# Kernel tuning notes

Measured on AMD Instinct MI355X. Metric: run time of the kernel, lower is better.

## Reference

```python
import jax, jax.numpy as jnp
import numpy as np

N, E, D, H, O = 100000, 1600000, 128, 128, 64
EPS = 1e-5


def setup_inputs() -> dict:
    key = jax.random.key(0)
    ks = jax.random.split(key, 12)
    s = 0.05
    return {
        "x": jax.random.normal(ks[0], (N, D), jnp.float32),
        "edge_index": jax.random.randint(ks[1], (2, E), 0, N),
        "W1": jax.random.normal(ks[2], (D, H), jnp.float32) * s,
        "b1": jnp.zeros((H,), jnp.float32),
        "W2": jax.random.normal(ks[3], (H, H), jnp.float32) * s,
        "b2": jnp.zeros((H,), jnp.float32),
        "W3": jax.random.normal(ks[4], (H, H), jnp.float32) * s,
        "b3": jnp.zeros((H,), jnp.float32),
        "g1": jnp.ones((H,), jnp.float32),
        "be1": jnp.zeros((H,), jnp.float32),
        "g2": jnp.ones((H,), jnp.float32),
        "be2": jnp.zeros((H,), jnp.float32),
        "Wp1": jax.random.normal(ks[5], (H, H), jnp.float32) * s,
        "bp1": jnp.zeros((H,), jnp.float32),
        "Wp2": jax.random.normal(ks[6], (H, O), jnp.float32) * s,
        "bp2": jnp.zeros((O,), jnp.float32),
    }


def _layer_norm(h, g, b):
    mu = jnp.mean(h, axis=-1, keepdims=True)
    var = jnp.mean(jnp.square(h - mu), axis=-1, keepdims=True)
    return g * (h - mu) * jax.lax.rsqrt(var + EPS) + b


def reference(x, edge_index, W1, b1, W2, b2, W3, b3, g1, be1, g2, be2, Wp1, bp1, Wp2, bp2):
    n = x.shape[0]
    loop = jnp.arange(n)
    # GCN: add self-loops, symmetric normalization D^-1/2 (A+I) D^-1/2
    src = jnp.concatenate([edge_index[0], loop])
    dst = jnp.concatenate([edge_index[1], loop])
    deg = jax.ops.segment_sum(jnp.ones_like(src, x.dtype), dst, num_segments=n)
    dinv = jax.lax.rsqrt(jnp.maximum(deg, 1e-12))
    norm = dinv[src] * dinv[dst]  # [E+N]

    def gcn_conv(h, W, b):
        hw = h @ W                              # transform first (PyG GCNConv)
        msg = hw[src] * norm[:, None]           # gather + edge scale
        return jax.ops.segment_sum(msg, dst, num_segments=n) + b  # scatter-add

    # dropout is a no-op in eval mode
    h = _layer_norm(jax.nn.relu(gcn_conv(x, W1, b1)), g1, be1)
    h = _layer_norm(jax.nn.relu(gcn_conv(h, W2, b2)), g2, be2)
    h = jax.nn.relu(gcn_conv(h, W3, b3))
    h = h @ Wp1 + bp1
    h = h @ Wp2 + bp2
    return jax.nn.sigmoid(h)
```

## Files before the change

kernel.cpp:

```cpp
#include <hip/hip_runtime.h>
#include <hip/hip_bf16.h>

typedef __attribute__((ext_vector_type(8))) short short8;
typedef __attribute__((ext_vector_type(4))) float floatx4;
typedef unsigned int u32;

__device__ __forceinline__ u32 f2bf(float f) {
    union { float f; u32 u; } c; c.f = f;
    return (c.u + 0x7FFFu + ((c.u >> 16) & 1u)) >> 16;
}

__device__ __forceinline__ void fp8x8_acc(uint2 v, float* a) {
    auto f0 = __builtin_amdgcn_cvt_pk_f32_fp8((int)v.x, false);
    auto f1 = __builtin_amdgcn_cvt_pk_f32_fp8((int)v.x, true);
    auto f2 = __builtin_amdgcn_cvt_pk_f32_fp8((int)v.y, false);
    auto f3 = __builtin_amdgcn_cvt_pk_f32_fp8((int)v.y, true);
    a[0] += ((const float*)&f0)[0]; a[1] += ((const float*)&f0)[1];
    a[2] += ((const float*)&f1)[0]; a[3] += ((const float*)&f1)[1];
    a[4] += ((const float*)&f2)[0]; a[5] += ((const float*)&f2)[1];
    a[6] += ((const float*)&f3)[0]; a[7] += ((const float*)&f3)[1];
}
__device__ __forceinline__ void fp8x8_dec(uint2 v, float* x) {
    auto f0 = __builtin_amdgcn_cvt_pk_f32_fp8((int)v.x, false);
    auto f1 = __builtin_amdgcn_cvt_pk_f32_fp8((int)v.x, true);
    auto f2 = __builtin_amdgcn_cvt_pk_f32_fp8((int)v.y, false);
    auto f3 = __builtin_amdgcn_cvt_pk_f32_fp8((int)v.y, true);
    x[0] = ((const float*)&f0)[0]; x[1] = ((const float*)&f0)[1];
    x[2] = ((const float*)&f1)[0]; x[3] = ((const float*)&f1)[1];
    x[4] = ((const float*)&f2)[0]; x[5] = ((const float*)&f2)[1];
    x[6] = ((const float*)&f3)[0]; x[7] = ((const float*)&f3)[1];
}
__device__ __forceinline__ u32 f32x4_to_fp8(float a, float b, float c, float d) {
    u32 w = (u32)__builtin_amdgcn_cvt_pk_fp8_f32(a, b, 0, false);
    w = (u32)__builtin_amdgcn_cvt_pk_fp8_f32(c, d, (int)w, true);
    return w;
}

#define CCAP 264
#define CAPB 8192

__device__ __forceinline__ void gatherq(const uint2* __restrict__ hw64,
                                        const int* __restrict__ col,
                                        int* __restrict__ ldsc,
                                        int begq, int endq, int beg, int stagelen,
                                        int lane, int s16, float* __restrict__ acc) {
    for (int i = lane; i < stagelen; i += 64) ldsc[i] = col[beg + i];
    __syncthreads();
    int dq = endq - begq;
    int offq = begq - beg;
    int send = min(endq, beg + stagelen);
    int sdq = max(0, send - begq);
    int mx = sdq;
    mx = max(mx, __shfl_xor(mx, 16));
    mx = max(mx, __shfl_xor(mx, 32));
    for (int jb = 0; jb < mx; jb += 8) {
        uint2 v[8];
#pragma unroll
        for (int j = 0; j < 8; ++j) {
            int jj = jb + j;
            int cj = ldsc[min(offq + jj, CCAP - 1)];
            bool act = jj < sdq;
            uint2 tv; tv.x = 0u; tv.y = 0u;
            if (act) tv = hw64[(size_t)cj * 16 + s16];
            v[j] = tv;
        }
#pragma unroll
        for (int j = 0; j < 8; ++j) fp8x8_acc(v[j], acc);
    }
    for (int j = sdq; j < dq; ++j) {
        int cj = col[begq + j];
        uint2 tv = hw64[(size_t)cj * 16 + s16];
        fp8x8_acc(tv, acc);
    }
}

__global__ __launch_bounds__(256) void bucket_trans_k(
        const int* __restrict__ src, const int* __restrict__ dst,
        int* __restrict__ gcnt, u32* __restrict__ pairs, int E, int nb, int bucketB,
        const float* __restrict__ W1, const float* __restrict__ W2,
        const float* __restrict__ W3, const float* __restrict__ Wp1,
        const float* __restrict__ Wp2,
        unsigned short* __restrict__ o1, unsigned short* __restrict__ o2,
        unsigned short* __restrict__ o3, unsigned short* __restrict__ o4,
        unsigned short* __restrict__ o5) {
    int t = threadIdx.x;
    if ((int)blockIdx.x >= bucketB) {
        int i = (blockIdx.x - bucketB) * 256 + t;
        const float* in; unsigned short* out; int cols, li;
        if (i < 16384)      { in = W1;  out = o1; cols = 128; li = i; }
        else if (i < 32768) { in = W2;  out = o2; cols = 128; li = i - 16384; }
        else if (i < 49152) { in = W3;  out = o3; cols = 128; li = i - 32768; }
        else if (i < 65536) { in = Wp1; out = o4; cols = 128; li = i - 49152; }
        else                { in = Wp2; out = o5; cols = 64;  li = i - 65536; }
        int r = li / cols, c = li - r * cols;
        out[(size_t)c * 128 + r] = (unsigned short)f2bf(in[li]);
        return;
    }
    __shared__ int cnt[512];
    __shared__ int gbase[512];
    __shared__ int cur[512];
    cnt[t] = 0; cnt[t + 256] = 0;
    __syncthreads();
    int e0 = blockIdx.x * 8192;
    int ne = min(8192, E - e0);
    for (int i = t; i < ne; i += 256) atomicAdd(&cnt[dst[e0 + i] >> 8], 1);
    __syncthreads();
    for (int b = t; b < nb; b += 256) {
        int c = cnt[b];
        gbase[b] = c ? (b * CAPB + atomicAdd(&gcnt[b], c)) : 0;
        cur[b] = 0;
    }
    __syncthreads();
    for (int i = t; i < ne; i += 256) {
        int d = dst[e0 + i];
        int s = src[e0 + i];
        int b = d >> 8;
        int p = atomicAdd(&cur[b], 1);
        pairs[gbase[b] + p] = (u32)s | ((u32)(d & 255) << 24);
    }
}

#define LCOL_CAP 12288
__global__ __launch_bounds__(256) void build_k(const u32* __restrict__ pairs,
                                               const int* __restrict__ gcnt,
                                               int* __restrict__ rowptr,
                                               float* __restrict__ dinv,
                                               int* __restrict__ col,
                                               int N, int E, int nb) {
    __shared__ int pre[512];
    __shared__ int cnt[256], incl[256], cur[256];
    __shared__ int lcol[LCOL_CAP];
    int b = blockIdx.x, t = threadIdx.x;
    pre[t] = (t < nb) ? gcnt[t] : 0;
    pre[t + 256] = (t + 256 < nb) ? gcnt[t + 256] : 0;
    __syncthreads();
    for (int off = 1; off < 512; off <<= 1) {
        int a0 = (t >= off) ? pre[t - off] : 0;
        int a1 = (t + 256 >= off) ? pre[t + 256 - off] : 0;
        __syncthreads();
        pre[t] += a0;
        pre[t + 256] += a1;
        __syncthreads();
    }
    int myg = gcnt[b];
    int base = pre[b] - myg;
    int sbase = b * CAPB;
    int ecnt = myg;
    cnt[t] = 0;
    __syncthreads();
    for (int j = t; j < ecnt; j += 256) atomicAdd(&cnt[pairs[sbase + j] >> 24], 1);
    __syncthreads();
    incl[t] = cnt[t];
    __syncthreads();
    for (int off = 1; off < 256; off <<= 1) {
        int a = (t >= off) ? incl[t - off] : 0;
        __syncthreads();
        incl[t] += a;
        __syncthreads();
    }
    int myc = cnt[t];
    int ex = incl[t] - myc;
    int node = b * 256 + t;
    if (node < N) {
        rowptr[node] = base + ex;
        dinv[node] = rsqrtf((float)myc + 1.0f);
    }
    cur[t] = ex;
    if (b == 0 && t == 0) rowptr[N] = E;
    __syncthreads();
    if (ecnt <= LCOL_CAP) {
        for (int j = t; j < ecnt; j += 256) {
            u32 v = pairs[sbase + j];
            int r = atomicAdd(&cur[v >> 24], 1);
            lcol[r] = (int)(v & 0xFFFFFF);
        }
        __syncthreads();
        for (int j = t; j < ecnt; j += 256) col[base + j] = lcol[j];
    } else {
        for (int j = t; j < ecnt; j += 256) {
            u32 v = pairs[sbase + j];
            int r = atomicAdd(&cur[v >> 24], 1);
            col[base + r] = (int)(v & 0xFFFFFF);
        }
    }
}

__global__ __launch_bounds__(256) void gemm1_k(const float* __restrict__ A,
                                               const short* __restrict__ Wt,
                                               const float* __restrict__ dinv,
                                               u32* __restrict__ out, int M) {
    __shared__ unsigned short xs[64][132];
    int t = threadIdx.x;
    int wave = t >> 6, lane = t & 63;
    int r0 = blockIdx.x * 64;
#pragma unroll
    for (int i = 0; i < 8; ++i) {
        int idx = i * 256 + t;
        int row = idx >> 5;
        int c4 = idx & 31;
        int grow = r0 + row;
        float4 f = {0.f, 0.f, 0.f, 0.f};
        if (grow < M) f = ((const float4*)A)[(size_t)grow * 32 + c4];
        uint2 bb;
        bb.x = f2bf(f.x) | (f2bf(f.y) << 16);
        bb.y = f2bf(f.z) | (f2bf(f.w) << 16);
        *(uint2*)&xs[row][c4 * 4] = bb;
    }
    __syncthreads();
    int m0 = r0 + wave * 16;
    if (m0 >= M) return;
    int quad = lane >> 4, lr = lane & 15;
    int lrow = wave * 16 + lr;
    int row = m0 + lr;
    bool wr = row < M;
    short8 b0 = *(const short8*)&xs[lrow][quad * 8];
    short8 b1 = *(const short8*)&xs[lrow][32 + quad * 8];
    short8 b2 = *(const short8*)&xs[lrow][64 + quad * 8];
    short8 b3 = *(const short8*)&xs[lrow][96 + quad * 8];
    float di = wr ? dinv[row] : 0.f;
#pragma unroll
    for (int nt = 0; nt < 8; ++nt) {
        int ncol = nt * 16 + lr;
        const short8* Wp = (const short8*)(Wt + (size_t)ncol * 128 + quad * 8);
        short8 a0 = Wp[0], a1 = Wp[4], a2 = Wp[8], a3 = Wp[12];
        floatx4 acc = {0.f, 0.f, 0.f, 0.f};
        acc = __builtin_amdgcn_mfma_f32_16x16x32_bf16(a0, b0, acc, 0, 0, 0);
        acc = __builtin_amdgcn_mfma_f32_16x16x32_bf16(a1, b1, acc, 0, 0, 0);
        acc = __builtin_amdgcn_mfma_f32_16x16x32_bf16(a2, b2, acc, 0, 0, 0);
        acc = __builtin_amdgcn_mfma_f32_16x16x32_bf16(a3, b3, acc, 0, 0, 0);
        if (wr) {
            out[(size_t)row * 32 + nt * 4 + quad] =
                f32x4_to_fp8(acc[0] * di, acc[1] * di, acc[2] * di, acc[3] * di);
        }
    }
}

__global__ __launch_bounds__(256) void fconv_k(const uint2* __restrict__ hw64,
                                               const int* __restrict__ rowptr,
                                               const int* __restrict__ col,
                                               const float* __restrict__ dinv,
                                               const float* __restrict__ bias,
                                               const float* __restrict__ gam,
                                               const float* __restrict__ bet,
                                               const short* __restrict__ Wt,
                                               u32* __restrict__ out, int N) {
    __shared__ unsigned short rows[16][136];
    __shared__ int ldsc[4][CCAP];
    int t = threadIdx.x, wave = t >> 6, lane = t & 63;
    int q = lane >> 4, s16 = lane & 15;
    int nb0 = blockIdx.x * 16;
    int node0 = nb0 + wave * 4;
    int node = node0 + q;
    bool ok = node < N;
    int beg = rowptr[min(node0, N)];
    int e4  = rowptr[min(node0 + 4, N)];
    int begq = rowptr[min(node, N)];
    int endq = ok ? rowptr[min(node + 1, N)] : begq;
    int stagelen = min(e4 - beg, 256);
    uint2 selfd; selfd.x = 0u; selfd.y = 0u;
    float di = 0.f;
    if (ok) {
        selfd = hw64[(size_t)node * 16 + s16];
        di = dinv[node];
    }
    float acc[8] = {0.f, 0.f, 0.f, 0.f, 0.f, 0.f, 0.f, 0.f};
    gatherq(hw64, col, ldsc[wave], begq, endq, beg, stagelen, lane, s16, acc);

    float sx[8]; fp8x8_dec(selfd, sx);
    float4 bv0 = *(const float4*)(bias + 8 * s16);
    float4 bv1 = *(const float4*)(bias + 8 * s16 + 4);
    float a[8];
    a[0] = fmaxf(di * (acc[0] + sx[0]) + bv0.x, 0.f);
    a[1] = fmaxf(di * (acc[1] + sx[1]) + bv0.y, 0.f);
    a[2] = fmaxf(di * (acc[2] + sx[2]) + bv0.z, 0.f);
    a[3] = fmaxf(di * (acc[3] + sx[3]) + bv0.w, 0.f);
    a[4] = fmaxf(di * (acc[4] + sx[4]) + bv1.x, 0.f);
    a[5] = fmaxf(di * (acc[5] + sx[5]) + bv1.y, 0.f);
    a[6] = fmaxf(di * (acc[6] + sx[6]) + bv1.z, 0.f);
    a[7] = fmaxf(di * (acc[7] + sx[7]) + bv1.w, 0.f);
    if (!ok) {
#pragma unroll
        for (int k = 0; k < 8; ++k) a[k] = 0.f;
    }
    float s = 0.f, qq = 0.f;
#pragma unroll
    for (int k = 0; k < 8; ++k) { s += a[k]; qq += a[k] * a[k]; }
#pragma unroll
    for (int mm = 8; mm >= 1; mm >>= 1) {
        s += __shfl_xor(s, mm);
        qq += __shfl_xor(qq, mm);
    }
    float mu = s * (1.f / 128.f);
    float var = qq * (1.f / 128.f) - mu * mu;
    float rs = rsqrtf(fmaxf(var, 0.f) + 1e-5f);
    float4 gv0 = *(const float4*)(gam + 8 * s16);
    float4 gv1 = *(const float4*)(gam + 8 * s16 + 4);
    float4 be0 = *(const float4*)(bet + 8 * s16);
    float4 be1 = *(const float4*)(bet + 8 * s16 + 4);
    a[0] = gv0.x * (a[0] - mu) * rs + be0.x;
    a[1] = gv0.y * (a[1] - mu) * rs + be0.y;
    a[2] = gv0.z * (a[2] - mu) * rs + be0.z;
    a[3] = gv0.w * (a[3] - mu) * rs + be0.w;
    a[4] = gv1.x * (a[4] - mu) * rs + be1.x;
    a[5] = gv1.y * (a[5] - mu) * rs + be1.y;
    a[6] = gv1.z * (a[6] - mu) * rs + be1.z;
    a[7] = gv1.w * (a[7] - mu) * rs + be1.w;
    if (!ok) {
#pragma unroll
        for (int k = 0; k < 8; ++k) a[k] = 0.f;
    }
    int r = wave * 4 + q;
    uint4 st;
    st.x = f2bf(a[0]) | (f2bf(a[1]) << 16);
    st.y = f2bf(a[2]) | (f2bf(a[3]) << 16);
    st.z = f2bf(a[4]) | (f2bf(a[5]) << 16);
    st.w = f2bf(a[6]) | (f2bf(a[7]) << 16);
    *(uint4*)((char*)&rows[r][0] + 16 * s16) = st;
    __syncthreads();

    int quad = lane >> 4, lr = lane & 15;
    short8 b0 = *(const short8*)&rows[lr][quad * 8];
    short8 b1 = *(const short8*)&rows[lr][32 + quad * 8];
    short8 b2 = *(const short8*)&rows[lr][64 + quad * 8];
    short8 b3 = *(const short8*)&rows[lr][96 + quad * 8];
    int onode = nb0 + lr;
    float di2 = (onode < N) ? dinv[onode] : 0.f;
#pragma unroll
    for (int k = 0; k < 2; ++k) {
        int ct = wave * 2 + k;
        int ncol = ct * 16 + lr;
        const short8* Wp = (const short8*)(Wt + (size_t)ncol * 128 + quad * 8);
        short8 a0 = Wp[0], a1 = Wp[4], a2 = Wp[8], a3 = Wp[12];
        floatx4 acm = {0.f, 0.f, 0.f, 0.f};
        acm = __builtin_amdgcn_mfma_f32_16x16x32_bf16(a0, b0, acm, 0, 0, 0);
        acm = __builtin_amdgcn_mfma_f32_16x16x32_bf16(a1, b1, acm, 0, 0, 0);
        acm = __builtin_amdgcn_mfma_f32_16x16x32_bf16(a2, b2, acm, 0, 0, 0);
        acm = __builtin_amdgcn_mfma_f32_16x16x32_bf16(a3, b3, acm, 0, 0, 0);
        int c0 = ct * 16 + quad * 4;
        if (onode < N) {
            out[(size_t)onode * 32 + (c0 >> 2)] =
                f32x4_to_fp8(acm[0] * di2, acm[1] * di2, acm[2] * di2, acm[3] * di2);
        }
    }
}

__global__ __launch_bounds__(256) void fhead_k(const uint2* __restrict__ hw64,
                                               const int* __restrict__ rowptr,
                                               const int* __restrict__ col,
                                               const float* __restrict__ dinv,
                                               const float* __restrict__ bias,
                                               const short* __restrict__ Wp1t,
                                               const float* __restrict__ bp1,
                                               const short* __restrict__ Wp2t,
                                               const float* __restrict__ bp2,
                                               float* __restrict__ out, int N) {
    __shared__ unsigned short rows[16][136];
    __shared__ unsigned short h1s[16][136];
    __shared__ int ldsc[4][CCAP];
    int t = threadIdx.x, wave = t >> 6, lane = t & 63;
    int q = lane >> 4, s16 = lane & 15;
    int nb0 = blockIdx.x * 16;
    int node0 = nb0 + wave * 4;
    int node = node0 + q;
    bool ok = node < N;
    int beg = rowptr[min(node0, N)];
    int e4  = rowptr[min(node0 + 4, N)];
    int begq = rowptr[min(node, N)];
    int endq = ok ? rowptr[min(node + 1, N)] : begq;
    int stagelen = min(e4 - beg, 256);
    uint2 selfd; selfd.x = 0u; selfd.y = 0u;
    float di = 0.f;
    if (ok) {
        selfd = hw64[(size_t)node * 16 + s16];
        di = dinv[node];
    }
    float acc[8] = {0.f, 0.f, 0.f, 0.f, 0.f, 0.f, 0.f, 0.f};
    gatherq(hw64, col, ldsc[wave], begq, endq, beg, stagelen, lane, s16, acc);

    float sx[8]; fp8x8_dec(selfd, sx);
    float4 bv0 = *(const float4*)(bias + 8 * s16);
    float4 bv1 = *(const float4*)(bias + 8 * s16 + 4);
    float a[8];
    a[0] = fmaxf(di * (acc[0] + sx[0]) + bv0.x, 0.f);
    a[1] = fmaxf(di * (acc[1] + sx[1]) + bv0.y, 0.f);
    a[2] = fmaxf(di * (acc[2] + sx[2]) + bv0.z, 0.f);
    a[3] = fmaxf(di * (acc[3] + sx[3]) + bv0.w, 0.f);
    a[4] = fmaxf(di * (acc[4] + sx[4]) + bv1.x, 0.f);
    a[5] = fmaxf(di * (acc[5] + sx[5]) + bv1.y, 0.f);
    a[6] = fmaxf(di * (acc[6] + sx[6]) + bv1.z, 0.f);
    a[7] = fmaxf(di * (acc[7] + sx[7]) + bv1.w, 0.f);
    if (!ok) {
#pragma unroll
        for (int k = 0; k < 8; ++k) a[k] = 0.f;
    }
    int r = wave * 4 + q;
    uint4 st;
    st.x = f2bf(a[0]) | (f2bf(a[1]) << 16);
    st.y = f2bf(a[2]) | (f2bf(a[3]) << 16);
    st.z = f2bf(a[4]) | (f2bf(a[5]) << 16);
    st.w = f2bf(a[6]) | (f2bf(a[7]) << 16);
    *(uint4*)((char*)&rows[r][0] + 16 * s16) = st;
    __syncthreads();

    int quad = lane >> 4, lr = lane & 15;
    {
        short8 b0 = *(const short8*)&rows[lr][quad * 8];
        short8 b1 = *(const short8*)&rows[lr][32 + quad * 8];
        short8 b2 = *(const short8*)&rows[lr][64 + quad * 8];
        short8 b3 = *(const short8*)&rows[lr][96 + quad * 8];
#pragma unroll
        for (int k = 0; k < 2; ++k) {
            int ct = wave * 2 + k;
            int ncol = ct * 16 + lr;
            const short8* Wp = (const short8*)(Wp1t + (size_t)ncol * 128 + quad * 8);
            short8 a0 = Wp[0], a1 = Wp[4], a2 = Wp[8], a3 = Wp[12];
            floatx4 acm = {0.f, 0.f, 0.f, 0.f};
            acm = __builtin_amdgcn_mfma_f32_16x16x32_bf16(a0, b0, acm, 0, 0, 0);
            acm = __builtin_amdgcn_mfma_f32_16x16x32_bf16(a1, b1, acm, 0, 0, 0);
            acm = __builtin_amdgcn_mfma_f32_16x16x32_bf16(a2, b2, acm, 0, 0, 0);
            acm = __builtin_amdgcn_mfma_f32_16x16x32_bf16(a3, b3, acm, 0, 0, 0);
            int c0 = ct * 16 + quad * 4;
            float4 bv = *(const float4*)(bp1 + c0);
            uint2 stq;
            stq.x = f2bf(acm[0] + bv.x) | (f2bf(acm[1] + bv.y) << 16);
            stq.y = f2bf(acm[2] + bv.z) | (f2bf(acm[3] + bv.w) << 16);
            *(uint2*)&h1s[lr][c0] = stq;
        }
    }
    __syncthreads();
    {
        short8 b0 = *(const short8*)&h1s[lr][quad * 8];
        short8 b1 = *(const short8*)&h1s[lr][32 + quad * 8];
        short8 b2 = *(const short8*)&h1s[lr][64 + quad * 8];
        short8 b3 = *(const short8*)&h1s[lr][96 + quad * 8];
        int ncol = wave * 16 + lr;
        const short8* Wp = (const short8*)(Wp2t + (size_t)ncol * 128 + quad * 8);
        short8 a0 = Wp[0], a1 = Wp[4], a2 = Wp[8], a3 = Wp[12];
        floatx4 acm = {0.f, 0.f, 0.f, 0.f};
        acm = __builtin_amdgcn_mfma_f32_16x16x32_bf16(a0, b0, acm, 0, 0, 0);
        acm = __builtin_amdgcn_mfma_f32_16x16x32_bf16(a1, b1, acm, 0, 0, 0);
        acm = __builtin_amdgcn_mfma_f32_16x16x32_bf16(a2, b2, acm, 0, 0, 0);
        acm = __builtin_amdgcn_mfma_f32_16x16x32_bf16(a3, b3, acm, 0, 0, 0);
        int c0 = wave * 16 + quad * 4;
        int onode = nb0 + lr;
        if (onode < N) {
            float4 bv = *(const float4*)(bp2 + c0);
            float4 sg;
            sg.x = 1.f / (1.f + __expf(-(acm[0] + bv.x)));
            sg.y = 1.f / (1.f + __expf(-(acm[1] + bv.y)));
            sg.z = 1.f / (1.f + __expf(-(acm[2] + bv.z)));
            sg.w = 1.f / (1.f + __expf(-(acm[3] + bv.w)));
            *(float4*)(out + (size_t)onode * 64 + c0) = sg;
        }
    }
}

extern "C" void kernel_launch(void* const* d_in, const int* in_sizes, int n_in,
                              void* d_out, int out_size, void* d_ws, size_t ws_size,
                              hipStream_t stream) {
    const int N = in_sizes[0] / 128;
    const int E = in_sizes[1] / 2;
    const int nb = (N + 255) >> 8;
    const int* edge = (const int*)d_in[1];
    const int* srcp = edge;
    const int* dstp = edge + E;
    const float* x   = (const float*)d_in[0];
    const float* W1  = (const float*)d_in[2];
    const float* b1  = (const float*)d_in[3];
    const float* W2  = (const float*)d_in[4];
    const float* b2  = (const float*)d_in[5];
    const float* W3  = (const float*)d_in[6];
    const float* b3  = (const float*)d_in[7];
    const float* g1  = (const float*)d_in[8];
    const float* be1 = (const float*)d_in[9];
    const float* g2  = (const float*)d_in[10];
    const float* be2 = (const float*)d_in[11];
    const float* Wp1 = (const float*)d_in[12];
    const float* bp1 = (const float*)d_in[13];
    const float* Wp2 = (const float*)d_in[14];
    const float* bp2 = (const float*)d_in[15];

    char* ws = (char*)d_ws;
    size_t off = 0;
    auto alloc = [&](size_t b) -> char* {
        char* p = ws + off;
        off += (b + 255) & ~(size_t)255;
        return p;
    };
    int* gcnt   = (int*)alloc(512 * 4);
    int* rowptr = (int*)alloc((size_t)(N + 1) * 4);
    float* dinv = (float*)alloc((size_t)N * 4);
    u32* pairs  = (u32*)alloc((size_t)nb * CAPB * 4);
    int* colA   = (int*)alloc((size_t)E * 4);
    unsigned char* hw  = (unsigned char*)alloc((size_t)N * 128);
    unsigned char* hb  = (unsigned char*)alloc((size_t)N * 128);
    unsigned short* w1t = (unsigned short*)alloc(128 * 128 * 2);
    unsigned short* w2t = (unsigned short*)alloc(128 * 128 * 2);
    unsigned short* w3t = (unsigned short*)alloc(128 * 128 * 2);
    unsigned short* wp1t = (unsigned short*)alloc(128 * 128 * 2);
    unsigned short* wp2t = (unsigned short*)alloc(64 * 128 * 2);
    if (off > ws_size) return;

    int gb = (N + 63) / 64;
    int fb = (N + 15) / 16;
    int bucketB = (E + 8191) / 8192;

    hipMemsetAsync(gcnt, 0, 512 * 4, stream);
    bucket_trans_k<<<bucketB + 288, 256, 0, stream>>>(srcp, dstp, gcnt, pairs, E, nb,
                                                      bucketB, W1, W2, W3, Wp1, Wp2,
                                                      w1t, w2t, w3t, wp1t, wp2t);
    build_k<<<nb, 256, 0, stream>>>(pairs, gcnt, rowptr, dinv, colA, N, E, nb);

    gemm1_k<<<gb, 256, 0, stream>>>(x, (const short*)w1t, dinv, (u32*)hw, N);
    fconv_k<<<fb, 256, 0, stream>>>((const uint2*)hw, rowptr, colA, dinv,
                                    b1, g1, be1, (const short*)w2t, (u32*)hb, N);
    fconv_k<<<fb, 256, 0, stream>>>((const uint2*)hb, rowptr, colA, dinv,
                                    b2, g2, be2, (const short*)w3t, (u32*)hw, N);
    fhead_k<<<fb, 256, 0, stream>>>((const uint2*)hw, rowptr, colA, dinv, b3,
                                    (const short*)wp1t, bp1, (const short*)wp2t, bp2,
                                    (float*)d_out, N);
}
```

Before: 361.2 us.

## Fuse all GCN stages into one persistent cooperative kernel with grid syncs

Replaces the memset plus six separate kernel launches with a single cooperative persistent kernel. Each block loops over the stages' tiles and a grid-wide barrier separates the stages, with shared memory taken from one dynamic pool. The aim is to remove per-launch overhead and the gaps between kernels. In exchange the grid is capped by occupancy, so each block must loop over many tiles, launch bounds of 4 blocks per CU may limit registers, and the local column capacity in the build stage shrinks from 12288 to 8192 entries.

```diff
diff --git a/kernel.cpp b/kernel.cpp
--- a/kernel.cpp
+++ b/kernel.cpp
@@ -1,5 +1,8 @@
 #include <hip/hip_runtime.h>
 #include <hip/hip_bf16.h>
+#include <hip/hip_cooperative_groups.h>
+
+namespace cg = cooperative_groups;
 
 typedef __attribute__((ext_vector_type(8))) short short8;
 typedef __attribute__((ext_vector_type(4))) float floatx4;
@@ -38,6 +41,21 @@
 
 #define CCAP 264
 #define CAPB 8192
+#define LCOL_CAP 8192
+#define POOL_BYTES 37888
+
+struct P {
+    const int* src; const int* dst;
+    int* gcnt; u32* pairs;
+    int* rowptr; float* dinv; int* col;
+    const float* x;
+    const float *W1, *W2, *W3, *Wp1, *Wp2;
+    const float *b1, *b2, *b3, *g1, *be1, *g2, *be2, *bp1, *bp2;
+    unsigned short *w1t, *w2t, *w3t, *wp1t, *wp2t;
+    u32 *hw, *hb;
+    float* out;
+    int N, E, nb, bucketB, gb, fb;
+};
 
 __device__ __forceinline__ void gatherq(const uint2* __restrict__ hw64,
                                         const int* __restrict__ col,
@@ -74,65 +92,53 @@
     }
 }
 
-__global__ __launch_bounds__(256) void bucket_trans_k(
-        const int* __restrict__ src, const int* __restrict__ dst,
-        int* __restrict__ gcnt, u32* __restrict__ pairs, int E, int nb, int bucketB,
-        const float* __restrict__ W1, const float* __restrict__ W2,
-        const float* __restrict__ W3, const float* __restrict__ Wp1,
-        const float* __restrict__ Wp2,
-        unsigned short* __restrict__ o1, unsigned short* __restrict__ o2,
-        unsigned short* __restrict__ o3, unsigned short* __restrict__ o4,
-        unsigned short* __restrict__ o5) {
-    int t = threadIdx.x;
-    if ((int)blockIdx.x >= bucketB) {
-        int i = (blockIdx.x - bucketB) * 256 + t;
+__device__ void dev_bucket_trans(const P& p, int ci, int t, char* pool) {
+    if (ci >= p.bucketB) {
+        int i = (ci - p.bucketB) * 256 + t;
         const float* in; unsigned short* out; int cols, li;
-        if (i < 16384)      { in = W1;  out = o1; cols = 128; li = i; }
-        else if (i < 32768) { in = W2;  out = o2; cols = 128; li = i - 16384; }
-        else if (i < 49152) { in = W3;  out = o3; cols = 128; li = i - 32768; }
-        else if (i < 65536) { in = Wp1; out = o4; cols = 128; li = i - 49152; }
-        else                { in = Wp2; out = o5; cols = 64;  li = i - 65536; }
+        if (i < 16384)      { in = p.W1;  out = p.w1t;  cols = 128; li = i; }
+        else if (i < 32768) { in = p.W2;  out = p.w2t;  cols = 128; li = i - 16384; }
+        else if (i < 49152) { in = p.W3;  out = p.w3t;  cols = 128; li = i - 32768; }
+        else if (i < 65536) { in = p.Wp1; out = p.wp1t; cols = 128; li = i - 49152; }
+        else                { in = p.Wp2; out = p.wp2t; cols = 64;  li = i - 65536; }
         int r = li / cols, c = li - r * cols;
         out[(size_t)c * 128 + r] = (unsigned short)f2bf(in[li]);
         return;
     }
-    __shared__ int cnt[512];
-    __shared__ int gbase[512];
-    __shared__ int cur[512];
+    int* cnt   = (int*)pool;
+    int* gbase = cnt + 512;
+    int* cur   = gbase + 512;
+    __syncthreads();
     cnt[t] = 0; cnt[t + 256] = 0;
     __syncthreads();
-    int e0 = blockIdx.x * 8192;
-    int ne = min(8192, E - e0);
-    for (int i = t; i < ne; i += 256) atomicAdd(&cnt[dst[e0 + i] >> 8], 1);
-    __syncthreads();
-    for (int b = t; b < nb; b += 256) {
+    int e0 = ci * 8192;
+    int ne = min(8192, p.E - e0);
+    for (int i = t; i < ne; i += 256) atomicAdd(&cnt[p.dst[e0 + i] >> 8], 1);
+    __syncthreads();
+    for (int b = t; b < p.nb; b += 256) {
         int c = cnt[b];
-        gbase[b] = c ? (b * CAPB + atomicAdd(&gcnt[b], c)) : 0;
+        gbase[b] = c ? (b * CAPB + atomicAdd(&p.gcnt[b], c)) : 0;
         cur[b] = 0;
     }
     __syncthreads();
     for (int i = t; i < ne; i += 256) {
-        int d = dst[e0 + i];
-        int s = src[e0 + i];
+        int d = p.dst[e0 + i];
+        int s = p.src[e0 + i];
         int b = d >> 8;
-        int p = atomicAdd(&cur[b], 1);
-        pairs[gbase[b] + p] = (u32)s | ((u32)(d & 255) << 24);
-    }
-}
-
-#define LCOL_CAP 12288
-__global__ __launch_bounds__(256) void build_k(const u32* __restrict__ pairs,
-                                               const int* __restrict__ gcnt,
-                                               int* __restrict__ rowptr,
-                                               float* __restrict__ dinv,
-                                               int* __restrict__ col,
-                                               int N, int E, int nb) {
-    __shared__ int pre[512];
-    __shared__ int cnt[256], incl[256], cur[256];
-    __shared__ int lcol[LCOL_CAP];
-    int b = blockIdx.x, t = threadIdx.x;
-    pre[t] = (t < nb) ? gcnt[t] : 0;
-    pre[t + 256] = (t + 256 < nb) ? gcnt[t + 256] : 0;
+        int pp = atomicAdd(&cur[b], 1);
+        p.pairs[gbase[b] + pp] = (u32)s | ((u32)(d & 255) << 24);
+    }
+}
+
+__device__ void dev_build(const P& p, int b, int t, char* pool) {
+    int* pre  = (int*)pool;
+    int* cnt  = pre + 512;
+    int* incl = cnt + 256;
+    int* cur  = incl + 256;
+    int* lcol = cur + 256;
+    __syncthreads();
+    pre[t] = (t < p.nb) ? p.gcnt[t] : 0;
+    pre[t + 256] = (t + 256 < p.nb) ? p.gcnt[t + 256] : 0;
     __syncthreads();
     for (int off = 1; off < 512; off <<= 1) {
         int a0 = (t >= off) ? pre[t - off] : 0;
@@ -142,13 +148,13 @@
         pre[t + 256] += a1;
         __syncthreads();
     }
-    int myg = gcnt[b];
+    int myg = p.gcnt[b];
     int base = pre[b] - myg;
     int sbase = b * CAPB;
     int ecnt = myg;
     cnt[t] = 0;
     __syncthreads();
-    for (int j = t; j < ecnt; j += 256) atomicAdd(&cnt[pairs[sbase + j] >> 24], 1);
+    for (int j = t; j < ecnt; j += 256) atomicAdd(&cnt[p.pairs[sbase + j] >> 24], 1);
     __syncthreads();
     incl[t] = cnt[t];
     __syncthreads();
@@ -161,46 +167,44 @@
     int myc = cnt[t];
     int ex = incl[t] - myc;
     int node = b * 256 + t;
-    if (node < N) {
-        rowptr[node] = base + ex;
-        dinv[node] = rsqrtf((float)myc + 1.0f);
+    if (node < p.N) {
+        p.rowptr[node] = base + ex;
+        p.dinv[node] = rsqrtf((float)myc + 1.0f);
     }
     cur[t] = ex;
-    if (b == 0 && t == 0) rowptr[N] = E;
+    if (b == 0 && t == 0) p.rowptr[p.N] = p.E;
     __syncthreads();
     if (ecnt <= LCOL_CAP) {
         for (int j = t; j < ecnt; j += 256) {
-            u32 v = pairs[sbase + j];
+            u32 v = p.pairs[sbase + j];
             int r = atomicAdd(&cur[v >> 24], 1);
             lcol[r] = (int)(v & 0xFFFFFF);
         }
         __syncthreads();
-        for (int j = t; j < ecnt; j += 256) col[base + j] = lcol[j];
+        for (int j = t; j < ecnt; j += 256) p.col[base + j] = lcol[j];
     } else {
         for (int j = t; j < ecnt; j += 256) {
-            u32 v = pairs[sbase + j];
+            u32 v = p.pairs[sbase + j];
             int r = atomicAdd(&cur[v >> 24], 1);
-            col[base + r] = (int)(v & 0xFFFFFF);
-        }
-    }
-}
-
-__global__ __launch_bounds__(256) void gemm1_k(const float* __restrict__ A,
-                                               const short* __restrict__ Wt,
-                                               const float* __restrict__ dinv,
-                                               u32* __restrict__ out, int M) {
-    __shared__ unsigned short xs[64][132];
-    int t = threadIdx.x;
+            p.col[base + r] = (int)(v & 0xFFFFFF);
+        }
+    }
+}
+
+__device__ void dev_gemm1(const P& p, int tile, int t, char* pool) {
+    typedef unsigned short row132[132];
+    row132* xs = (row132*)pool;
+    __syncthreads();
     int wave = t >> 6, lane = t & 63;
-    int r0 = blockIdx.x * 64;
+    int r0 = tile * 64;
+    int M = p.N;
 #pragma unroll
     for (int i = 0; i < 8; ++i) {
         int idx = i * 256 + t;
-        int row = idx >> 5;
-        int c4 = idx & 31;
+        int row = idx >> 5, c4 = idx & 31;
         int grow = r0 + row;
         float4 f = {0.f, 0.f, 0.f, 0.f};
-        if (grow < M) f = ((const float4*)A)[(size_t)grow * 32 + c4];
+        if (grow < M) f = ((const float4*)p.x)[(size_t)grow * 32 + c4];
         uint2 bb;
         bb.x = f2bf(f.x) | (f2bf(f.y) << 16);
         bb.y = f2bf(f.z) | (f2bf(f.w) << 16);
@@ -217,7 +221,8 @@
     short8 b1 = *(const short8*)&xs[lrow][32 + quad * 8];
     short8 b2 = *(const short8*)&xs[lrow][64 + quad * 8];
     short8 b3 = *(const short8*)&xs[lrow][96 + quad * 8];
-    float di = wr ? dinv[row] : 0.f;
+    float di = wr ? p.dinv[row] : 0.f;
+    const short* Wt = (const short*)p.w1t;
 #pragma unroll
     for (int nt = 0; nt < 8; ++nt) {
         int ncol = nt * 16 + lr;
@@ -229,26 +234,25 @@
         acc = __builtin_amdgcn_mfma_f32_16x16x32_bf16(a2, b2, acc, 0, 0, 0);
         acc = __builtin_amdgcn_mfma_f32_16x16x32_bf16(a3, b3, acc, 0, 0, 0);
         if (wr) {
-            out[(size_t)row * 32 + nt * 4 + quad] =
+            p.hw[(size_t)row * 32 + nt * 4 + quad] =
                 f32x4_to_fp8(acc[0] * di, acc[1] * di, acc[2] * di, acc[3] * di);
         }
     }
 }
 
-__global__ __launch_bounds__(256) void fconv_k(const uint2* __restrict__ hw64,
-                                               const int* __restrict__ rowptr,
-                                               const int* __restrict__ col,
-                                               const float* __restrict__ dinv,
-                                               const float* __restrict__ bias,
-                                               const float* __restrict__ gam,
-                                               const float* __restrict__ bet,
-                                               const short* __restrict__ Wt,
-                                               u32* __restrict__ out, int N) {
-    __shared__ unsigned short rows[16][136];
-    __shared__ int ldsc[4][CCAP];
-    int t = threadIdx.x, wave = t >> 6, lane = t & 63;
+__device__ void dev_fconv(const uint2* __restrict__ hw64,
+                          const int* __restrict__ rowptr, const int* __restrict__ col,
+                          const float* __restrict__ dinv, const float* __restrict__ bias,
+                          const float* __restrict__ gam, const float* __restrict__ bet,
+                          const short* __restrict__ Wt, u32* __restrict__ out,
+                          int N, int tile, int t, char* pool) {
+    typedef unsigned short row136[136];
+    row136* rows = (row136*)pool;
+    int (*ldsc)[CCAP] = (int(*)[CCAP])(pool + 4352);
+    __syncthreads();
+    int wave = t >> 6, lane = t & 63;
     int q = lane >> 4, s16 = lane & 15;
-    int nb0 = blockIdx.x * 16;
+    int nb0 = tile * 16;
     int node0 = nb0 + wave * 4;
     int node = node0 + q;
     bool ok = node < N;
@@ -344,22 +348,20 @@
     }
 }
 
-__global__ __launch_bounds__(256) void fhead_k(const uint2* __restrict__ hw64,
-                                               const int* __restrict__ rowptr,
-                                               const int* __restrict__ col,
-                                               const float* __restrict__ dinv,
-                                               const float* __restrict__ bias,
-                                               const short* __restrict__ Wp1t,
-                                               const float* __restrict__ bp1,
-                                               const short* __restrict__ Wp2t,
-                                               const float* __restrict__ bp2,
-                                               float* __restrict__ out, int N) {
-    __shared__ unsigned short rows[16][136];
-    __shared__ unsigned short h1s[16][136];
-    __shared__ int ldsc[4][CCAP];
-    int t = threadIdx.x, wave = t >> 6, lane = t & 63;
+__device__ void dev_fhead(const uint2* __restrict__ hw64,
+                          const int* __restrict__ rowptr, const int* __restrict__ col,
+                          const float* __restrict__ dinv, const float* __restrict__ bias,
+                          const short* __restrict__ Wp1t, const float* __restrict__ bp1,
+                          const short* __restrict__ Wp2t, const float* __restrict__ bp2,
+                          float* __restrict__ out, int N, int tile, int t, char* pool) {
+    typedef unsigned short row136[136];
+    row136* rows = (row136*)pool;
+    row136* h1s  = (row136*)(pool + 4352);
+    int (*ldsc)[CCAP] = (int(*)[CCAP])(pool + 8704);
+    __syncthreads();
+    int wave = t >> 6, lane = t & 63;
     int q = lane >> 4, s16 = lane & 15;
-    int nb0 = blockIdx.x * 16;
+    int nb0 = tile * 16;
     int node0 = nb0 + wave * 4;
     int node = node0 + q;
     bool ok = node < N;
@@ -455,6 +457,70 @@
     }
 }
 
+__global__ __launch_bounds__(256, 4) void mega_k(P p) {
+    extern __shared__ __align__(16) char smem[];
+    cg::grid_group g = cg::this_grid();
+    int t = threadIdx.x;
+    for (int i = blockIdx.x * 256 + t; i < 512; i += gridDim.x * 256) p.gcnt[i] = 0;
+    __threadfence();
+    g.sync();
+    for (int c = blockIdx.x; c < p.bucketB + 288; c += gridDim.x)
+        dev_bucket_trans(p, c, t, smem);
+    __threadfence();
+    g.sync();
+    for (int b = blockIdx.x; b < p.nb; b += gridDim.x)
+        dev_build(p, b, t, smem);
+    __threadfence();
+    g.sync();
+    for (int tb = blockIdx.x; tb < p.gb; tb += gridDim.x)
+        dev_gemm1(p, tb, t, smem);
+    __threadfence();
+    g.sync();
+    for (int tb = blockIdx.x; tb < p.fb; tb += gridDim.x)
+        dev_fconv((const uint2*)p.hw, p.rowptr, p.col, p.dinv, p.b1, p.g1, p.be1,
+                  (const short*)p.w2t, p.hb, p.N, tb, t, smem);
+    __threadfence();
+    g.sync();
+    for (int tb = blockIdx.x; tb < p.fb; tb += gridDim.x)
+        dev_fconv((const uint2*)p.hb, p.rowptr, p.col, p.dinv, p.b2, p.g2, p.be2,
+                  (const short*)p.w3t, p.hw, p.N, tb, t, smem);
+    __threadfence();
+    g.sync();
+    for (int tb = blockIdx.x; tb < p.fb; tb += gridDim.x)
+        dev_fhead((const uint2*)p.hw, p.rowptr, p.col, p.dinv, p.b3,
+                  (const short*)p.wp1t, p.bp1, (const short*)p.wp2t, p.bp2,
+                  p.out, p.N, tb, t, smem);
+}
+
+__global__ __launch_bounds__(256) void bucket_trans_k(P p) {
+    extern __shared__ __align__(16) char smem[];
+    dev_bucket_trans(p, blockIdx.x, threadIdx.x, smem);
+}
+__global__ __launch_bounds__(256) void build_k(P p) {
+    extern __shared__ __align__(16) char smem[];
+    dev_build(p, blockIdx.x, threadIdx.x, smem);
+}
+__global__ __launch_bounds__(256) void gemm1_k(P p) {
+    extern __shared__ __align__(16) char smem[];
+    dev_gemm1(p, blockIdx.x, threadIdx.x, smem);
+}
+__global__ __launch_bounds__(256) void fconv1_k(P p) {
+    extern __shared__ __align__(16) char smem[];
+    dev_fconv((const uint2*)p.hw, p.rowptr, p.col, p.dinv, p.b1, p.g1, p.be1,
+              (const short*)p.w2t, p.hb, p.N, blockIdx.x, threadIdx.x, smem);
+}
+__global__ __launch_bounds__(256) void fconv2_k(P p) {
+    extern __shared__ __align__(16) char smem[];
+    dev_fconv((const uint2*)p.hb, p.rowptr, p.col, p.dinv, p.b2, p.g2, p.be2,
+              (const short*)p.w3t, p.hw, p.N, blockIdx.x, threadIdx.x, smem);
+}
+__global__ __launch_bounds__(256) void fhead_k(P p) {
+    extern __shared__ __align__(16) char smem[];
+    dev_fhead((const uint2*)p.hw, p.rowptr, p.col, p.dinv, p.b3,
+              (const short*)p.wp1t, p.bp1, (const short*)p.wp2t, p.bp2,
+              p.out, p.N, blockIdx.x, threadIdx.x, smem);
+}
+
 extern "C" void kernel_launch(void* const* d_in, const int* in_sizes, int n_in,
                               void* d_out, int out_size, void* d_ws, size_t ws_size,
                               hipStream_t stream) {
@@ -462,23 +528,6 @@
     const int E = in_sizes[1] / 2;
     const int nb = (N + 255) >> 8;
     const int* edge = (const int*)d_in[1];
-    const int* srcp = edge;
-    const int* dstp = edge + E;
-    const float* x   = (const float*)d_in[0];
-    const float* W1  = (const float*)d_in[2];
-    const float* b1  = (const float*)d_in[3];
-    const float* W2  = (const float*)d_in[4];
-    const float* b2  = (const float*)d_in[5];
-    const float* W3  = (const float*)d_in[6];
-    const float* b3  = (const float*)d_in[7];
-    const float* g1  = (const float*)d_in[8];
-    const float* be1 = (const float*)d_in[9];
-    const float* g2  = (const float*)d_in[10];
-    const float* be2 = (const float*)d_in[11];
-    const float* Wp1 = (const float*)d_in[12];
-    const float* bp1 = (const float*)d_in[13];
-    const float* Wp2 = (const float*)d_in[14];
-    const float* bp2 = (const float*)d_in[15];
 
     char* ws = (char*)d_ws;
     size_t off = 0;
@@ -487,36 +536,64 @@
         off += (b + 255) & ~(size_t)255;
         return p;
     };
-    int* gcnt   = (int*)alloc(512 * 4);
-    int* rowptr = (int*)alloc((size_t)(N + 1) * 4);
-    float* dinv = (float*)alloc((size_t)N * 4);
-    u32* pairs  = (u32*)alloc((size_t)nb * CAPB * 4);
-    int* colA   = (int*)alloc((size_t)E * 4);
-    unsigned char* hw  = (unsigned char*)alloc((size_t)N * 128);
-    unsigned char* hb  = (unsigned char*)alloc((size_t)N * 128);
-    unsigned short* w1t = (unsigned short*)alloc(128 * 128 * 2);
-    unsigned short* w2t = (unsigned short*)alloc(128 * 128 * 2);
-    unsigned short* w3t = (unsigned short*)alloc(128 * 128 * 2);
-    unsigned short* wp1t = (unsigned short*)alloc(128 * 128 * 2);
-    unsigned short* wp2t = (unsigned short*)alloc(64 * 128 * 2);
+    P p;
+    p.src = edge;
+    p.dst = edge + E;
+    p.x   = (const float*)d_in[0];
+    p.W1  = (const float*)d_in[2];  p.b1  = (const float*)d_in[3];
+    p.W2  = (const float*)d_in[4];  p.b2  = (const float*)d_in[5];
+    p.W3  = (const float*)d_in[6];  p.b3  = (const float*)d_in[7];
+    p.g1  = (const float*)d_in[8];  p.be1 = (const float*)d_in[9];
+    p.g2  = (const float*)d_in[10]; p.be2 = (const float*)d_in[11];
+    p.Wp1 = (const float*)d_in[12]; p.bp1 = (const float*)d_in[13];
+    p.Wp2 = (const float*)d_in[14]; p.bp2 = (const float*)d_in[15];
+    p.gcnt   = (int*)alloc(512 * 4);
+    p.rowptr = (int*)alloc((size_t)(N + 1) * 4);
+    p.dinv   = (float*)alloc((size_t)N * 4);
+    p.pairs  = (u32*)alloc((size_t)nb * CAPB * 4);
+    p.col    = (int*)alloc((size_t)E * 4);
+    p.hw     = (u32*)alloc((size_t)N * 128);
+    p.hb     = (u32*)alloc((size_t)N * 128);
+    p.w1t  = (unsigned short*)alloc(128 * 128 * 2);
+    p.w2t  = (unsigned short*)alloc(128 * 128 * 2);
+    p.w3t  = (unsigned short*)alloc(128 * 128 * 2);
+    p.wp1t = (unsigned short*)alloc(128 * 128 * 2);
+    p.wp2t = (unsigned short*)alloc(64 * 128 * 2);
+    p.out = (float*)d_out;
+    p.N = N; p.E = E; p.nb = nb;
+    p.bucketB = (E + 8191) / 8192;
+    p.gb = (N + 63) / 64;
+    p.fb = (N + 15) / 16;
     if (off > ws_size) return;
 
-    int gb = (N + 63) / 64;
-    int fb = (N + 15) / 16;
-    int bucketB = (E + 8191) / 8192;
-
-    hipMemsetAsync(gcnt, 0, 512 * 4, stream);
-    bucket_trans_k<<<bucketB + 288, 256, 0, stream>>>(srcp, dstp, gcnt, pairs, E, nb,
-                                                      bucketB, W1, W2, W3, Wp1, Wp2,
-                                                      w1t, w2t, w3t, wp1t, wp2t);
-    build_k<<<nb, 256, 0, stream>>>(pairs, gcnt, rowptr, dinv, colA, N, E, nb);
-
-    gemm1_k<<<gb, 256, 0, stream>>>(x, (const short*)w1t, dinv, (u32*)hw, N);
-    fconv_k<<<fb, 256, 0, stream>>>((const uint2*)hw, rowptr, colA, dinv,
-                                    b1, g1, be1, (const short*)w2t, (u32*)hb, N);
-    fconv_k<<<fb, 256, 0, stream>>>((const uint2*)hb, rowptr, colA, dinv,
-                                    b2, g2, be2, (const short*)w3t, (u32*)hw, N);
-    fhead_k<<<fb, 256, 0, stream>>>((const uint2*)hw, rowptr, colA, dinv, b3,
-                                    (const short*)wp1t, bp1, (const short*)wp2t, bp2,
-                                    (float*)d_out, N);
-}
+    static int s_grid = -1;
+    if (s_grid < 0) {
+        hipDeviceProp_t prop{};
+        if (hipGetDeviceProperties(&prop, 0) == hipSuccess && prop.cooperativeLaunch) {
+            int mb = 0;
+            if (hipOccupancyMaxActiveBlocksPerMultiprocessor(&mb, mega_k, 256,
+                                                             (size_t)POOL_BYTES) != hipSuccess ||
+                mb < 1)
+                mb = 4;
+            if (mb > 8) mb = 8;
+            s_grid = mb * prop.multiProcessorCount;
+        } else {
+            s_grid = 0;
+        }
+    }
+
+    if (s_grid > 0) {
+        void* args[] = {(void*)&p};
+        hipLaunchCooperativeKernel((const void*)mega_k, dim3(s_grid), dim3(256),
+                                   args, POOL_BYTES, stream);
+        return;
+    }
+
+    hipMemsetAsync(p.gcnt, 0, 512 * 4, stream);
+    bucket_trans_k<<<p.bucketB + 288, 256, 6144, stream>>>(p);
+    build_k<<<p.nb, 256, POOL_BYTES, stream>>>(p);
+    gemm1_k<<<p.gb, 256, 16896, stream>>>(p);
+    fconv1_k<<<p.fb, 256, 8576, stream>>>(p);
+    fconv2_k<<<p.fb, 256, 8576, stream>>>(p);
+    fhead_k<<<p.fb, 256, 12928, stream>>>(p);
+}
```

Result: slower. 1.008 ms (+179.1%).
